# Performance work log

Hardware: AMD Instinct MI355X
Metric: run time of the kernel (lower is better)

## Reference

```python
import jax, jax.numpy as jnp
import numpy as np

B, T, META = 2, 1024, 6
VOCAB, MVOCAB = 32000, 1000
D, H, L = 512, 8, 6
HS = D // H          # 64
T1 = T + META        # 1030
CHUNK = 6            # sliding/chunk granularity hard-coded in generate_matrix
LN_EPS = 1e-5


def _layernorm(x, g, b):
    mu = jnp.mean(x, axis=-1, keepdims=True)
    var = jnp.mean((x - mu) ** 2, axis=-1, keepdims=True)
    return (x - mu) * jax.lax.rsqrt(var + LN_EPS) * g + b


def _pos_encoding(t, d):
    # torch: sin((position // 6) * div_term), cos(...) interleaved even/odd
    pos = jnp.floor(jnp.arange(t, dtype=jnp.float32) / CHUNK)
    div = jnp.exp(jnp.arange(0, d, 2, dtype=jnp.float32) * (-np.log(10000.0) / d))
    ang = pos[:, None] * div[None, :]                     # [t, d/2]
    enc = jnp.zeros((t, d), dtype=jnp.float32)
    enc = enc.at[:, 0::2].set(jnp.sin(ang))
    enc = enc.at[:, 1::2].set(jnp.cos(ang))
    return enc


def _mask(n):
    # row i attends to cols [0, (i//6+1)*6) plus the last 6 (metadata) cols
    r = jnp.arange(n)
    return (r[None, :] < (r[:, None] // CHUNK + 1) * CHUNK) | (r[None, :] >= n - CHUNK)


def setup_inputs() -> dict:
    key = jax.random.key(0)
    ks = jax.random.split(key, 16)
    s = 0.02
    n = lambda k, shp: jax.random.normal(k, shp, dtype=jnp.float32) * s
    return {
        "idx": jax.random.randint(ks[0], (B, T), 0, VOCAB),
        "metadata_idx": jax.random.randint(ks[1], (B, META), 0, MVOCAB),
        "tok_emb": n(ks[2], (VOCAB, D)),
        "meta_emb": n(ks[3], (MVOCAB, D)),
        "Wq": n(ks[4], (L, H, D, HS)),
        "Wk": n(ks[5], (L, H, D, HS)),
        "Wv": n(ks[6], (L, H, D, HS)),
        "Wo": n(ks[7], (L, D, D)),
        "bo": jnp.zeros((L, D), jnp.float32),
        "W1": n(ks[8], (L, D, 4 * D)),
        "b1": jnp.zeros((L, 4 * D), jnp.float32),
        "W2": n(ks[9], (L, 4 * D, D)),
        "b2": jnp.zeros((L, D), jnp.float32),
        "ln1_g": jnp.ones((L, D), jnp.float32),
        "ln1_b": jnp.zeros((L, D), jnp.float32),
        "ln2_g": jnp.ones((L, D), jnp.float32),
        "ln2_b": jnp.zeros((L, D), jnp.float32),
        "lnf_g": jnp.ones((D,), jnp.float32),
        "lnf_b": jnp.zeros((D,), jnp.float32),
        "Wlm": n(ks[10], (D, VOCAB)),
        "blm": jnp.zeros((VOCAB,), jnp.float32),
    }


def reference(idx, metadata_idx, tok_emb, meta_emb, Wq, Wk, Wv, Wo, bo,
              W1, b1, W2, b2, ln1_g, ln1_b, ln2_g, ln2_b, lnf_g, lnf_b, Wlm, blm):
    x = tok_emb[idx] + _pos_encoding(T, D)                 # [B, T, D]
    x = jnp.concatenate([x, meta_emb[metadata_idx]], axis=1)  # [B, T1, D]
    scale = D ** -0.5          # NOTE: original scales by full n_embd, not head_size
    mask = _mask(T1)
    neg_inf = jnp.float32(-jnp.inf)
    for l in range(L):
        h = _layernorm(x, ln1_g[l], ln1_b[l])
        q = jnp.einsum('btd,hde->bhte', h, Wq[l])          # [B, H, T1, HS]
        k = jnp.einsum('btd,hde->bhte', h, Wk[l])
        v = jnp.einsum('btd,hde->bhte', h, Wv[l])
        wei = jnp.einsum('bhqe,bhke->bhqk', q, k) * scale  # [B, H, T1, T1]
        wei = jnp.where(mask, wei, neg_inf)
        wei = jax.nn.softmax(wei, axis=-1)
        o = jnp.einsum('bhqk,bhke->bhqe', wei, v)          # [B, H, T1, HS]
        o = jnp.transpose(o, (0, 2, 1, 3)).reshape(x.shape[0], T1, D)
        x = x + o @ Wo[l] + bo[l]
        h = _layernorm(x, ln2_g[l], ln2_b[l])
        x = x + jax.nn.relu(h @ W1[l] + b1[l]) @ W2[l] + b2[l]
    x = _layernorm(x, lnf_g, lnf_b)
    logits = x @ Wlm + blm                                  # [B, T1, VOCAB]
    return logits[:, :T, :]
```

## Files before the change

### kernel.cpp

```cpp
#include <hip/hip_runtime.h>
#include <hip/hip_bf16.h>
#include <math.h>

#define TT     1024
#define METAN  6
#define TT1    1030
#define BB     2
#define DD     512
#define HH     8
#define HSZ    64
#define LL     6
#define NVOCAB 32000
#define MROWS  2060
#define MPAD   2176
#define SCALE  0.044194173824159216f
#define NPART  16

typedef float  f32x4  __attribute__((ext_vector_type(4)));
typedef __bf16 bf16x8 __attribute__((ext_vector_type(8)));

__device__ __forceinline__ __bf16 f2bf(float f) { return (__bf16)f; }

__device__ __forceinline__ void glds16(const __bf16* g, const __bf16* l) {
  __builtin_amdgcn_global_load_lds(
      (const __attribute__((address_space(1))) unsigned int*)g,
      (__attribute__((address_space(3))) unsigned int*)l, 16, 0, 0);
}

__device__ __forceinline__ bf16x8 ln8v(float4 v0, float4 v1, float mu, float rs,
                                       float4 g0, float4 g1, float4 b0, float4 b1) {
  float vv[8] = {v0.x, v0.y, v0.z, v0.w, v1.x, v1.y, v1.z, v1.w};
  float gg[8] = {g0.x, g0.y, g0.z, g0.w, g1.x, g1.y, g1.z, g1.w};
  float bb[8] = {b0.x, b0.y, b0.z, b0.w, b1.x, b1.y, b1.z, b1.w};
  bf16x8 r;
#pragma unroll
  for (int j = 0; j < 8; j++) r[j] = f2bf((vv[j] - mu) * rs * gg[j] + bb[j]);
  return r;
}
__device__ __forceinline__ bf16x8 ln8(const float* xp, float mu, float rs,
                                      const float* g, const float* b) {
  return ln8v(*(const float4*)xp, *(const float4*)(xp + 4), mu, rs,
              *(const float4*)g, *(const float4*)(g + 4),
              *(const float4*)b, *(const float4*)(b + 4));
}

__device__ __forceinline__ void row_stats(const float* ps, const float* pq, int row,
                                          float& mu, float& rs) {
  float s = 0.f, q = 0.f;
#pragma unroll
  for (int j = 0; j < NPART; j++) { s += ps[(size_t)row * NPART + j]; q += pq[(size_t)row * NPART + j]; }
  mu = s * (1.0f / 512.0f);
  rs = rsqrtf(fmaxf(q * (1.0f / 512.0f) - mu * mu, 0.f) + 1e-5f);
}

__global__ void k_lnpw(const float* x, const float* ps, const float* pq,
                       const float* g, const float* b, __bf16* xf)
{
  const int sub = threadIdx.x >> 6;
  const int lane = threadIdx.x & 63;
  int row = blockIdx.x * 4 + sub;
  int sr = (row >> 10) * TT1 + (row & 1023);
  float mu, rs;
  row_stats(ps, pq, sr, mu, rs);
  bf16x8 o = ln8(&x[(size_t)sr * DD + lane * 8], mu, rs, &g[lane * 8], &b[lane * 8]);
  *(bf16x8*)&xf[(size_t)row * DD + lane * 8] = o;
}

__global__ void k_tcvt8(const float* __restrict__ Wq, const float* __restrict__ Wk,
                        const float* __restrict__ Wv, const float* __restrict__ Wo,
                        const float* __restrict__ W1, const float* __restrict__ W2,
                        const float* __restrict__ Wlm,
                        __bf16* __restrict__ wqkvb, __bf16* __restrict__ wob,
                        __bf16* __restrict__ w1b, __bf16* __restrict__ w2b,
                        __bf16* __restrict__ wlmb,
                        const int* idx, const int* midx, const float* tok,
                        const float* met, float* x, float* ps, float* pq)
{
  int bid = blockIdx.x;
  if (bid >= 34432) {
    const int sub = threadIdx.x >> 7;
    const int tl  = threadIdx.x & 127;
    const int d0  = tl * 4;
    int row = (bid - 34432) * 2 + sub;
    int b = row / TT1, tk = row - b * TT1;
    float v[4];
    if (tk < TT) {
      const float* e = tok + (size_t)idx[b * TT + tk] * DD;
      float pos = (float)(tk / 6);
#pragma unroll
      for (int j = 0; j < 4; j += 2) {
        int i = (d0 + j) >> 1;
        float dv = expf((float)i * (-2.0f * 9.210340371976184f / 512.0f));
        float ang = pos * dv;
        v[j]     = e[d0 + j]     + sinf(ang);
        v[j + 1] = e[d0 + j + 1] + cosf(ang);
      }
    } else {
      const float* e = met + (size_t)midx[b * METAN + (tk - TT)] * DD;
#pragma unroll
      for (int j = 0; j < 4; j++) v[j] = e[d0 + j];
    }
    *(float4*)&x[(size_t)row * DD + d0] = *(float4*)v;
    float s = v[0] + v[1] + v[2] + v[3];
    float q = v[0]*v[0] + v[1]*v[1] + v[2]*v[2] + v[3]*v[3];
#pragma unroll
    for (int msk = 1; msk < 8; msk <<= 1) { s += __shfl_xor(s, msk); q += __shfl_xor(q, msk); }
    if ((tl & 7) == 0) {
      ps[(size_t)row * NPART + (tl >> 3)] = s;
      pq[(size_t)row * NPART + (tl >> 3)] = q;
    }
    return;
  }
  __shared__ float t[32][33];
  const float* in; __bf16* out;
  int gx, gy, C, R, lo_cnt, local;
  long long in_bs, bs_hi, bs_lo;
  if (bid < 4608) {
    int job = bid / 1536; local = bid - job * 1536;
    in = job == 0 ? Wq : (job == 1 ? Wk : Wv);
    out = wqkvb + (size_t)job * 262144;
    gx = 2; gy = 16; R = 512; C = 64; in_bs = 32768; bs_hi = 786432; bs_lo = 32768; lo_cnt = 8;
  } else if (bid < 6144) {
    local = bid - 4608; in = Wo; out = wob;
    gx = 16; gy = 16; R = 512; C = 512; in_bs = 262144; bs_hi = 262144; bs_lo = 0; lo_cnt = 1;
  } else if (bid < 12288) {
    local = bid - 6144; in = W1; out = w1b;
    gx = 64; gy = 16; R = 512; C = 2048; in_bs = 1048576; bs_hi = 1048576; bs_lo = 0; lo_cnt = 1;
  } else if (bid < 18432) {
    local = bid - 12288; in = W2; out = w2b;
    gx = 16; gy = 64; R = 2048; C = 512; in_bs = 1048576; bs_hi = 1048576; bs_lo = 0; lo_cnt = 1;
  } else {
    local = bid - 18432; in = Wlm; out = wlmb;
    gx = 1000; gy = 16; R = 512; C = 32000; in_bs = 0; bs_hi = 0; bs_lo = 0; lo_cnt = 1;
  }
  int bx = local % gx; int tmp = local / gx; int by = tmp % gy; int bz = tmp / gy;
  const float* ib = in + (long long)bz * in_bs;
  __bf16* ob = out + (long long)(bz / lo_cnt) * bs_hi + (long long)(bz % lo_cnt) * bs_lo;
  int tx = threadIdx.x & 31, ty = threadIdx.x >> 5;
  int c = bx * 32 + tx;
  for (int j = ty; j < 32; j += 8)
    t[j][tx] = ib[(size_t)(by * 32 + j) * C + c];
  __syncthreads();
  int r = by * 32 + tx;
  for (int j = ty; j < 32; j += 8)
    ob[(size_t)(bx * 32 + j) * R + r] = f2bf(t[tx][j]);
}

template <int MODE, bool RELU, bool BIAS, int AMODE, int MT, int NT, int WM, bool STAT, int KS>
__device__ __forceinline__ void gemm_tiles(
    unsigned char* smem,
    const __bf16* A, const float* Ax,
    const float* ps, const float* pq,
    const float* lng, const float* lnb,
    const __bf16* __restrict__ Bt, const float* bias,
    const float* res,
    float* outf, __bf16* outb,
    float* ops, float* opq,
    int M, int N, int K, int ntx, int nty)
{
  constexpr int WN  = 4 / WM;
  constexpr int WMS = MT / WM;
  constexpr int WNS = NT / WN;
  constexpr int MR  = WMS / 16;
  constexpr int NR  = WNS / 16;
  constexpr int RA  = MT / 32;
  constexpr int RB  = (NT + 31) / 32;

  __bf16* const Asm = (__bf16*)smem;
  __bf16* const Bsm = (__bf16*)smem + 2 * KS * MT * 64;

  const int tid = threadIdx.x;
  const int lane = tid & 63, w = tid >> 6;
  const int wm = (WN == 1) ? w : (w >> 1);
  const int wn = (WN == 1) ? 0 : (w & 1);
  const int rm = lane & 15, g4 = lane >> 4;
  const int nt = ntx * nty;

  int flat = blockIdx.x;
  { const int q = nt >> 3, rr = nt & 7; const int xcd = flat & 7, ii = flat >> 3;
    flat = (xcd < rr ? xcd * (q + 1) : rr * (q + 1) + (xcd - rr) * q) + ii; }
  const int row0 = (flat % ntx) * MT;
  const int col0 = (flat / ntx) * NT;

  f32x4 acc[MR][NR];
  const f32x4 fz = {0.f, 0.f, 0.f, 0.f};
#pragma unroll
  for (int i = 0; i < MR; i++)
#pragma unroll
    for (int j = 0; j < NR; j++) acc[i][j] = fz;

  const __bf16* bSrc[RB];
#pragma unroll
  for (int i = 0; i < RB; i++) {
    int c = i * 256 + (NT == 32 ? (tid & 255) : tid);
    int r = c >> 3; int j = (c & 7) ^ (r & 7);
    bSrc[i] = Bt + (size_t)(col0 + r) * K + j * 8;
  }
  const __bf16* aSrc[RA];
  const float *Ax0 = nullptr, *gk = nullptr, *bk = nullptr;
  float mu0 = 0.f, rs0 = 0.f;
  int oA0 = 0, oA1 = 0;
  if (AMODE == 0) {
#pragma unroll
    for (int i = 0; i < RA; i++) {
      int c = i * 256 + tid; int r = c >> 3; int j = (c & 7) ^ (r & 7);
      aSrc[i] = A + (size_t)(row0 + r) * K + j * 8;
    }
  } else {
    int srow = tid >> 2, skc = tid & 3;
    int sa0 = row0 + srow;
    Ax0 = Ax + (size_t)sa0 * DD + skc * 8;
    row_stats(ps, pq, sa0, mu0, rs0);
    gk = lng + skc * 8; bk = lnb + skc * 8;
    oA0 = (srow * 8 + (skc ^ (srow & 7))) * 8;
    oA1 = (srow * 8 + ((skc + 4) ^ (srow & 7))) * 8;
  }

  float4 xa0, xa1, xb0, xb1, ga0, ga1, gb0, gb1, ca0, ca1, cb0, cb1;
  auto loadA1 = [&](int k0) {
    xa0 = *(const float4*)(Ax0 + k0);      xa1 = *(const float4*)(Ax0 + k0 + 4);
    xb0 = *(const float4*)(Ax0 + k0 + 32); xb1 = *(const float4*)(Ax0 + k0 + 36);
    ga0 = *(const float4*)(gk + k0);       ga1 = *(const float4*)(gk + k0 + 4);
    gb0 = *(const float4*)(gk + k0 + 32);  gb1 = *(const float4*)(gk + k0 + 36);
    ca0 = *(const float4*)(bk + k0);       ca1 = *(const float4*)(bk + k0 + 4);
    cb0 = *(const float4*)(bk + k0 + 32);  cb1 = *(const float4*)(bk + k0 + 36);
  };
  auto writeA1 = [&](int buf) {
    __bf16* base = Asm + buf * KS * MT * 64;
    *(bf16x8*)(base + oA0) = ln8v(xa0, xa1, mu0, rs0, ga0, ga1, ca0, ca1);
    *(bf16x8*)(base + oA1) = ln8v(xb0, xb1, mu0, rs0, gb0, gb1, cb0, cb1);
  };
  auto stageB = [&](int buf, int k0) {
#pragma unroll
    for (int h = 0; h < KS; h++) {
      if (NT == 32) {
        glds16(bSrc[0] + k0 + h * 64, Bsm + (buf * KS + h) * NT * 64 + (tid & 255) * 8);
      } else {
#pragma unroll
        for (int i = 0; i < RB; i++)
          glds16(bSrc[i] + k0 + h * 64, Bsm + (buf * KS + h) * NT * 64 + (i * 256 + w * 64) * 8);
      }
    }
  };
  auto stageA0 = [&](int buf, int k0) {
#pragma unroll
    for (int h = 0; h < KS; h++)
#pragma unroll
      for (int i = 0; i < RA; i++)
        glds16(aSrc[i] + k0 + h * 64, Asm + (buf * KS + h) * MT * 64 + (i * 256 + w * 64) * 8);
  };

  stageB(0, 0);
  if (AMODE == 0) stageA0(0, 0);
  else { loadA1(0); writeA1(0); }
  __syncthreads();

  int cur = 0;
  const int BK = 64 * KS;
  for (int k0 = 0; k0 < K; k0 += BK) {
    const bool nxt = (k0 + BK < K);
    if (nxt) {
      stageB(cur ^ 1, k0 + BK);
      if (AMODE == 0) stageA0(cur ^ 1, k0 + BK);
      else loadA1(k0 + BK);
    }
#pragma unroll
    for (int h = 0; h < KS; h++) {
      const __bf16* Acur = Asm + (cur * KS + h) * MT * 64;
      const __bf16* Bcur = Bsm + (cur * KS + h) * NT * 64;
      bf16x8 af[MR][2], bf[NR][2];
#pragma unroll
      for (int m = 0; m < MR; m++) {
        int r = wm * WMS + m * 16 + rm;
        int c0 = r * 8 + (g4 ^ (r & 7));
        af[m][0] = *(const bf16x8*)(Acur + c0 * 8);
        af[m][1] = *(const bf16x8*)(Acur + (c0 ^ 4) * 8);
      }
#pragma unroll
      for (int n = 0; n < NR; n++) {
        int r = wn * WNS + n * 16 + rm;
        int c0 = r * 8 + (g4 ^ (r & 7));
        bf[n][0] = *(const bf16x8*)(Bcur + c0 * 8);
        bf[n][1] = *(const bf16x8*)(Bcur + (c0 ^ 4) * 8);
      }
#pragma unroll
      for (int t = 0; t < 2; t++)
#pragma unroll
        for (int m = 0; m < MR; m++)
#pragma unroll
          for (int n = 0; n < NR; n++)
            acc[m][n] = __builtin_amdgcn_mfma_f32_16x16x32_bf16(af[m][t], bf[n][t], acc[m][n], 0, 0, 0);
    }
    if (nxt) {
      if (AMODE == 1) writeA1(cur ^ 1);
      __syncthreads();
    }
    cur ^= 1;
  }

  if (MODE == 2) {
    __syncthreads();
    float* T = (float*)smem;
    const int wbase = w * (32 * 68);
    const int cg = lane & 15;
#pragma unroll
    for (int h = 0; h < MR / 2; h++) {
#pragma unroll
      for (int mm = 0; mm < 2; mm++) {
        int m = h * 2 + mm;
#pragma unroll
        for (int n = 0; n < NR; n++) {
          float bvv = BIAS ? bias[col0 + wn * WNS + n * 16 + rm] : 0.f;
#pragma unroll
          for (int r = 0; r < 4; r++)
            T[wbase + (mm * 16 + g4 * 4 + r) * 68 + n * 16 + rm] = acc[m][n][r] + bvv;
        }
      }
#pragma unroll
      for (int i = 0; i < 8; i++) {
        int rloc = g4 + i * 4;
        float4 v = *(float4*)&T[wbase + rloc * 68 + cg * 4];
        *(float4*)&outf[(size_t)(row0 + wm * WMS + h * 32 + rloc) * N + col0 + wn * WNS + cg * 4] = v;
      }
    }
  } else {
#pragma unroll
    for (int m = 0; m < MR; m++) {
      int row_b = row0 + wm * WMS + m * 16 + g4 * 4;
      float bv[NR];
#pragma unroll
      for (int n = 0; n < NR; n++) bv[n] = BIAS ? bias[col0 + wn * WNS + n * 16 + rm] : 0.f;
#pragma unroll
      for (int r = 0; r < 4; r++) {
        int row = row_b + r;
        float s = 0.f, qq = 0.f;
#pragma unroll
        for (int n = 0; n < NR; n++) {
          int col = col0 + wn * WNS + n * 16 + rm;
          float v = acc[m][n][r] + bv[n];
          if (MODE == 0) {
            if (RELU) v = fmaxf(v, 0.f);
            if (row < M) outb[(size_t)row * N + col] = f2bf(v);
          } else {
            if (row < M) { v += res[(size_t)row * N + col]; outf[(size_t)row * N + col] = v; }
            s += v; qq += v * v;
          }
        }
        if (MODE == 1 && STAT) {
#pragma unroll
          for (int msk = 1; msk < 16; msk <<= 1) { s += __shfl_xor(s, msk); qq += __shfl_xor(qq, msk); }
          if (rm == 0 && row < M) {
            ops[(size_t)row * NPART + (col0 >> 5)] = s;
            opq[(size_t)row * NPART + (col0 >> 5)] = qq;
          }
        }
      }
    }
  }
}

template <int MODE, bool RELU, bool BIAS, int AMODE, int MT, int NT, int WM, bool STAT>
__global__ __launch_bounds__(256, 3) void k_gemm(
    const __bf16* A, const float* Ax, const float* ps, const float* pq,
    const float* lng, const float* lnb,
    const __bf16* __restrict__ Bt, const float* bias, const float* res,
    float* outf, __bf16* outb, float* ops, float* opq,
    int M, int N, int K, int ntx, int nty)
{
  __shared__ __align__(16) unsigned char smem[(MT + NT) * 256];
  gemm_tiles<MODE, RELU, BIAS, AMODE, MT, NT, WM, STAT, 1>(
      smem, A, Ax, ps, pq, lng, lnb, Bt, bias, res, outf, outb, ops, opq,
      M, N, K, ntx, nty);
}

template <int MODE, bool RELU, bool BIAS, int MT, int NT, int WM, bool STAT>
__global__ __launch_bounds__(256, 3) void k_gemm2(
    const __bf16* A, const float* Ax, const float* ps, const float* pq,
    const float* lng, const float* lnb,
    const __bf16* __restrict__ Bt, const float* bias, const float* res,
    float* outf, __bf16* outb, float* ops, float* opq,
    int M, int N, int K, int ntx, int nty)
{
  __shared__ __align__(16) unsigned char smem[(MT + NT) * 512];
  gemm_tiles<MODE, RELU, BIAS, 0, MT, NT, WM, STAT, 2>(
      smem, A, Ax, ps, pq, lng, lnb, Bt, bias, res, outf, outb, ops, opq,
      M, N, K, ntx, nty);
}

template <int MODE, bool RELU, bool BIAS, int AMODE, int MT, int NT, int WM, bool STAT>
__global__ __launch_bounds__(256, 2) void k_gemmL(
    const __bf16* A, const float* Ax, const float* ps, const float* pq,
    const float* lng, const float* lnb,
    const __bf16* __restrict__ Bt, const float* bias, const float* res,
    float* outf, __bf16* outb, float* ops, float* opq,
    int M, int N, int K, int ntx, int nty)
{
  __shared__ __align__(16) unsigned char smem[(MT + NT) * 256];
  gemm_tiles<MODE, RELU, BIAS, AMODE, MT, NT, WM, STAT, 1>(
      smem, A, Ax, ps, pq, lng, lnb, Bt, bias, res, outf, outb, ops, opq,
      M, N, K, ntx, nty);
}

__global__ __launch_bounds__(256) void k_attnw(const __bf16* qkv, __bf16* ob)
{
  __shared__ __align__(16) __bf16 Ks[64][72];
  __shared__ __align__(16) __bf16 Vs[64][72];
  __shared__ __align__(16) __bf16 Ps[4][16][72];

  const int tid = threadIdx.x;
  const int lane = tid & 63, w = tid >> 6;
  const int rm = lane & 15, g4 = lane >> 4;
  const int skey = tid >> 3;
  const int shs = (tid & 7) * 8;
  const size_t rsd = 1536;
  const f32x4 fz = {0.f, 0.f, 0.f, 0.f};

  const int q_level = 16 - (blockIdx.x >> 4);
  const int bh = blockIdx.x & 15;
  const int b = bh >> 3, h = bh & 7;
  const int q0 = q_level * 64;
  const int qw = q0 + w * 16;

  const __bf16* qb = qkv + (size_t)b * TT1 * rsd + h * HSZ;
  const __bf16* kb = qb + 512;
  const __bf16* vb = qb + 1024;

  bf16x8 aq[2];
  {
    const __bf16* qp = qb + (size_t)(qw + rm) * rsd + 8 * g4;
    aq[0] = *(const bf16x8*)qp;
    aq[1] = *(const bf16x8*)(qp + 32);
  }

  int ae_[4];
#pragma unroll
  for (int r = 0; r < 4; r++) {
    int qr = qw + g4 * 4 + r;
    ae_[r] = (qr / 6 + 1) * 6;
  }

  float m_[4], l_[4];
  f32x4 accO[4];
#pragma unroll
  for (int j = 0; j < 4; j++) accO[j] = fz;
#pragma unroll
  for (int r = 0; r < 4; r++) { m_[r] = -1e30f; l_[r] = 0.f; }

  int aemax = ((q0 + 63) / 6 + 1) * 6;
  if (aemax > TT) aemax = TT;
  const int ntile = (aemax + 63) >> 6;

  for (int tt = 0; tt <= ntile; ++tt) {
    const bool meta = (tt == ntile);
    const int kt = meta ? TT : tt * 64;

    bf16x8 k0 = *(const bf16x8*)(kb + (size_t)(kt + skey) * rsd + shs);
    bf16x8 k1 = *(const bf16x8*)(kb + (size_t)(kt + skey + 32) * rsd + shs);
    bf16x8 v0 = *(const bf16x8*)(vb + (size_t)(kt + skey) * rsd + shs);
    bf16x8 v1 = *(const bf16x8*)(vb + (size_t)(kt + skey + 32) * rsd + shs);
    __syncthreads();
    *(bf16x8*)&Ks[skey][shs]      = k0;
    *(bf16x8*)&Ks[skey + 32][shs] = k1;
#pragma unroll
    for (int j = 0; j < 8; j++) {
      Vs[shs + j][skey]      = v0[j];
      Vs[shs + j][skey + 32] = v1[j];
    }
    __syncthreads();

    f32x4 s[4];
    __builtin_amdgcn_s_setprio(1);
#pragma unroll
    for (int nt2 = 0; nt2 < 4; nt2++) {
      f32x4 a = fz;
      bf16x8 bk0 = *(const bf16x8*)&Ks[nt2 * 16 + rm][8 * g4];
      bf16x8 bk1 = *(const bf16x8*)&Ks[nt2 * 16 + rm][32 + 8 * g4];
      a = __builtin_amdgcn_mfma_f32_16x16x32_bf16(aq[0], bk0, a, 0, 0, 0);
      a = __builtin_amdgcn_mfma_f32_16x16x32_bf16(aq[1], bk1, a, 0, 0, 0);
      s[nt2] = a;
    }
    __builtin_amdgcn_s_setprio(0);

    float alpha[4];
#pragma unroll
    for (int r = 0; r < 4; r++) {
      int lim = meta ? TT1 : ae_[r];
      float sv[4];
#pragma unroll
      for (int i = 0; i < 4; i++) {
        sv[i] = s[i][r] * SCALE;
        if (kt + i * 16 + rm >= lim) sv[i] = -1e30f;
      }
      float tm = fmaxf(fmaxf(sv[0], sv[1]), fmaxf(sv[2], sv[3]));
#pragma unroll
      for (int msk = 1; msk < 16; msk <<= 1) tm = fmaxf(tm, __shfl_xor(tm, msk));
      float mn = fmaxf(m_[r], tm);
      float pp[4]; float ts = 0.f;
#pragma unroll
      for (int i = 0; i < 4; i++) { pp[i] = __expf(sv[i] - mn); ts += pp[i]; }
#pragma unroll
      for (int msk = 1; msk < 16; msk <<= 1) ts += __shfl_xor(ts, msk);
      alpha[r] = __expf(m_[r] - mn);
      l_[r] = l_[r] * alpha[r] + ts;
      m_[r] = mn;
#pragma unroll
      for (int i = 0; i < 4; i++) Ps[w][g4 * 4 + r][rm + i * 16] = f2bf(pp[i]);
    }
#pragma unroll
    for (int j = 0; j < 4; j++)
#pragma unroll
      for (int r = 0; r < 4; r++) accO[j][r] *= alpha[r];
    __syncthreads();

    bf16x8 pa0 = *(const bf16x8*)&Ps[w][rm][8 * g4];
    bf16x8 pa1 = *(const bf16x8*)&Ps[w][rm][32 + 8 * g4];
    __builtin_amdgcn_s_setprio(1);
#pragma unroll
    for (int j = 0; j < 4; j++) {
      bf16x8 bv0 = *(const bf16x8*)&Vs[j * 16 + rm][8 * g4];
      bf16x8 bv1 = *(const bf16x8*)&Vs[j * 16 + rm][32 + 8 * g4];
      accO[j] = __builtin_amdgcn_mfma_f32_16x16x32_bf16(pa0, bv0, accO[j], 0, 0, 0);
      accO[j] = __builtin_amdgcn_mfma_f32_16x16x32_bf16(pa1, bv1, accO[j], 0, 0, 0);
    }
    __builtin_amdgcn_s_setprio(0);
  }

#pragma unroll
  for (int r = 0; r < 4; r++) {
    int q = qw + g4 * 4 + r;
    if (q < TT1) {
      float rl = 1.0f / l_[r];
#pragma unroll
      for (int j = 0; j < 4; j++)
        ob[((size_t)b * TT1 + q) * DD + h * HSZ + j * 16 + rm] = f2bf(accO[j][r] * rl);
    }
  }
}

extern "C" void kernel_launch(void* const* d_in, const int* in_sizes, int n_in,
                              void* d_out, int out_size, void* d_ws, size_t ws_size,
                              hipStream_t stream)
{
  const int*   idx   = (const int*)d_in[0];
  const int*   midx  = (const int*)d_in[1];
  const float* tok   = (const float*)d_in[2];
  const float* metae = (const float*)d_in[3];
  const float* Wq    = (const float*)d_in[4];
  const float* Wk    = (const float*)d_in[5];
  const float* Wv    = (const float*)d_in[6];
  const float* Wo    = (const float*)d_in[7];
  const float* bo    = (const float*)d_in[8];
  const float* W1    = (const float*)d_in[9];
  const float* b1    = (const float*)d_in[10];
  const float* W2    = (const float*)d_in[11];
  const float* b2    = (const float*)d_in[12];
  const float* ln1g  = (const float*)d_in[13];
  const float* ln1b  = (const float*)d_in[14];
  const float* ln2g  = (const float*)d_in[15];
  const float* ln2b  = (const float*)d_in[16];
  const float* lnfg  = (const float*)d_in[17];
  const float* lnfb  = (const float*)d_in[18];
  const float* Wlm   = (const float*)d_in[19];
  const float* blm   = (const float*)d_in[20];
  float* out = (float*)d_out;

  char* p = (char*)d_ws;
  auto alloc = [&](size_t bytes) { void* r = (void*)p; p += (bytes + 255) & ~(size_t)255; return r; };
  float*  x     = (float*)alloc((size_t)MPAD * 512 * 4);
  float*  ps_   = (float*)alloc((size_t)MPAD * NPART * 4);
  float*  pq_   = (float*)alloc((size_t)MPAD * NPART * 4);
  __bf16* qkv   = (__bf16*)alloc((size_t)MPAD * 1536 * 2);
  __bf16* obuf  = (__bf16*)alloc((size_t)MPAD * 512 * 2);
  __bf16* f1    = (__bf16*)alloc((size_t)MPAD * 2048 * 2);
  __bf16* xf    = (__bf16*)alloc((size_t)2048 * 512 * 2);
  __bf16* wqkvb = (__bf16*)alloc((size_t)6 * 1536 * 512 * 2);
  __bf16* wob   = (__bf16*)alloc((size_t)6 * 512 * 512 * 2);
  __bf16* w1b   = (__bf16*)alloc((size_t)6 * 2048 * 512 * 2);
  __bf16* w2b   = (__bf16*)alloc((size_t)6 * 512 * 2048 * 2);
  __bf16* wlmb  = (__bf16*)alloc((size_t)NVOCAB * 512 * 2);
  (void)in_sizes; (void)n_in; (void)out_size; (void)ws_size;

  k_tcvt8<<<dim3(35462), 256, 0, stream>>>(Wq, Wk, Wv, Wo, W1, W2, Wlm,
                                           wqkvb, wob, w1b, w2b, wlmb,
                                           idx, midx, tok, metae, x, ps_, pq_);

  for (int l = 0; l < LL; ++l) {
    k_gemm<0, false, false, 1, 64, 64, 4, false><<<dim3(816), 256, 0, stream>>>(
        nullptr, x, ps_, pq_, ln1g + l * 512, ln1b + l * 512,
        wqkvb + (size_t)l * 786432, nullptr, nullptr, nullptr, qkv,
        nullptr, nullptr, MROWS, 1536, 512, 34, 24);
    k_attnw<<<dim3(272), 256, 0, stream>>>(qkv, obuf);
    k_gemm2<1, false, true, 64, 32, 4, true><<<dim3(544), 256, 0, stream>>>(
        obuf, nullptr, nullptr, nullptr, nullptr, nullptr,
        wob + (size_t)l * 262144, bo + l * 512, x, x, nullptr,
        ps_, pq_, MROWS, 512, 512, 34, 16);
    k_gemm<0, true, true, 1, 64, 64, 4, false><<<dim3(1088), 256, 0, stream>>>(
        nullptr, x, ps_, pq_, ln2g + l * 512, ln2b + l * 512,
        w1b + (size_t)l * 1048576, b1 + l * 2048, nullptr, nullptr, f1,
        nullptr, nullptr, MROWS, 2048, 512, 34, 32);
    k_gemm2<1, false, true, 64, 32, 4, true><<<dim3(544), 256, 0, stream>>>(
        f1, nullptr, nullptr, nullptr, nullptr, nullptr,
        w2b + (size_t)l * 1048576, b2 + l * 512, x, x, nullptr,
        ps_, pq_, MROWS, 512, 2048, 34, 16);
  }

  k_lnpw<<<dim3(512), 256, 0, stream>>>(x, ps_, pq_, lnfg, lnfb, xf);
  k_gemmL<2, false, true, 0, 128, 128, 2, false><<<dim3(4000), 256, 0, stream>>>(
      xf, nullptr, nullptr, nullptr, nullptr, nullptr,
      wlmb, blm, nullptr, out, nullptr, nullptr, nullptr, 2048, NVOCAB, 512, 16, 250);
}
```

Baseline: 866.1 us.

## Double-buffer K/V tiles in attention kernel with register prefetch

The attention kernel now keeps two LDS buffers for K and V. It loads the next tile's K/V from global memory into registers before computing on the current tile, then writes them into the alternate buffer after the PV MFMAs. This lets the global load latency overlap with the QK and PV compute and cuts the barriers per tile from three to one. The barrier between writing and reading the per-wave P buffer is dropped, which relies on each wave using only its own Ps slice. The cost is double the LDS for K/V and more live registers, which could reduce occupancy.

Result: no change. 864.7 us (-0.2%).

```diff
diff --git a/kernel.cpp b/kernel.cpp
--- a/kernel.cpp
+++ b/kernel.cpp
@@ -403,8 +403,8 @@
 
 __global__ __launch_bounds__(256) void k_attnw(const __bf16* qkv, __bf16* ob)
 {
-  __shared__ __align__(16) __bf16 Ks[64][72];
-  __shared__ __align__(16) __bf16 Vs[64][72];
+  __shared__ __align__(16) __bf16 Ks[2][64][72];
+  __shared__ __align__(16) __bf16 Vs[2][64][72];
   __shared__ __align__(16) __bf16 Ps[4][16][72];
 
   const int tid = threadIdx.x;
@@ -450,31 +450,42 @@
   if (aemax > TT) aemax = TT;
   const int ntile = (aemax + 63) >> 6;
 
+  bf16x8 rk0, rk1, rv0, rv1;
+  auto kvload = [&](int kt) {
+    rk0 = *(const bf16x8*)(kb + (size_t)(kt + skey) * rsd + shs);
+    rk1 = *(const bf16x8*)(kb + (size_t)(kt + skey + 32) * rsd + shs);
+    rv0 = *(const bf16x8*)(vb + (size_t)(kt + skey) * rsd + shs);
+    rv1 = *(const bf16x8*)(vb + (size_t)(kt + skey + 32) * rsd + shs);
+  };
+  auto kvwrite = [&](int buf) {
+    *(bf16x8*)&Ks[buf][skey][shs]      = rk0;
+    *(bf16x8*)&Ks[buf][skey + 32][shs] = rk1;
+#pragma unroll
+    for (int j = 0; j < 8; j++) {
+      Vs[buf][shs + j][skey]      = rv0[j];
+      Vs[buf][shs + j][skey + 32] = rv1[j];
+    }
+  };
+  auto ktile = [&](int tt) { return (tt == ntile) ? TT : tt * 64; };
+
+  kvload(ktile(0));
+  kvwrite(0);
+  __syncthreads();
+
+  int cur = 0;
   for (int tt = 0; tt <= ntile; ++tt) {
     const bool meta = (tt == ntile);
-    const int kt = meta ? TT : tt * 64;
-
-    bf16x8 k0 = *(const bf16x8*)(kb + (size_t)(kt + skey) * rsd + shs);
-    bf16x8 k1 = *(const bf16x8*)(kb + (size_t)(kt + skey + 32) * rsd + shs);
-    bf16x8 v0 = *(const bf16x8*)(vb + (size_t)(kt + skey) * rsd + shs);
-    bf16x8 v1 = *(const bf16x8*)(vb + (size_t)(kt + skey + 32) * rsd + shs);
-    __syncthreads();
-    *(bf16x8*)&Ks[skey][shs]      = k0;
-    *(bf16x8*)&Ks[skey + 32][shs] = k1;
-#pragma unroll
-    for (int j = 0; j < 8; j++) {
-      Vs[shs + j][skey]      = v0[j];
-      Vs[shs + j][skey + 32] = v1[j];
-    }
-    __syncthreads();
+    const int kt = ktile(tt);
+    const bool nxt = (tt < ntile);
+    if (nxt) kvload(ktile(tt + 1));
 
     f32x4 s[4];
     __builtin_amdgcn_s_setprio(1);
 #pragma unroll
     for (int nt2 = 0; nt2 < 4; nt2++) {
       f32x4 a = fz;
-      bf16x8 bk0 = *(const bf16x8*)&Ks[nt2 * 16 + rm][8 * g4];
-      bf16x8 bk1 = *(const bf16x8*)&Ks[nt2 * 16 + rm][32 + 8 * g4];
+      bf16x8 bk0 = *(const bf16x8*)&Ks[cur][nt2 * 16 + rm][8 * g4];
+      bf16x8 bk1 = *(const bf16x8*)&Ks[cur][nt2 * 16 + rm][32 + 8 * g4];
       a = __builtin_amdgcn_mfma_f32_16x16x32_bf16(aq[0], bk0, a, 0, 0, 0);
       a = __builtin_amdgcn_mfma_f32_16x16x32_bf16(aq[1], bk1, a, 0, 0, 0);
       s[nt2] = a;
@@ -510,19 +521,24 @@
     for (int j = 0; j < 4; j++)
 #pragma unroll
       for (int r = 0; r < 4; r++) accO[j][r] *= alpha[r];
-    __syncthreads();
 
     bf16x8 pa0 = *(const bf16x8*)&Ps[w][rm][8 * g4];
     bf16x8 pa1 = *(const bf16x8*)&Ps[w][rm][32 + 8 * g4];
     __builtin_amdgcn_s_setprio(1);
 #pragma unroll
     for (int j = 0; j < 4; j++) {
-      bf16x8 bv0 = *(const bf16x8*)&Vs[j * 16 + rm][8 * g4];
-      bf16x8 bv1 = *(const bf16x8*)&Vs[j * 16 + rm][32 + 8 * g4];
+      bf16x8 bv0 = *(const bf16x8*)&Vs[cur][j * 16 + rm][8 * g4];
+      bf16x8 bv1 = *(const bf16x8*)&Vs[cur][j * 16 + rm][32 + 8 * g4];
       accO[j] = __builtin_amdgcn_mfma_f32_16x16x32_bf16(pa0, bv0, accO[j], 0, 0, 0);
       accO[j] = __builtin_amdgcn_mfma_f32_16x16x32_bf16(pa1, bv1, accO[j], 0, 0, 0);
     }
     __builtin_amdgcn_s_setprio(0);
+
+    if (nxt) {
+      kvwrite(cur ^ 1);
+      __syncthreads();
+    }
+    cur ^= 1;
   }
 
 #pragma unroll
```
